# Kernel optimization log

Hardware: AMD Instinct MI355X
Metric: run time of the kernel (lower is better)

The kernel has to match this reference:

```python
import jax, jax.numpy as jnp
import numpy as np

B, T, N, E = 32, 512, 4, 16          # batch, seq_len, num_nodes, num_edges (N*N)
NI, EI = 16, 8                        # node / edge input channels
HN, HE, MH, C = 128, 128, 256, 8      # hidden node/edge, mlp hidden, classes

# complete-graph edge list (matches the src/dst double loop in __init__)
SRC = np.repeat(np.arange(N), N)      # [E]
DST = np.tile(np.arange(N), N)        # [E]
# GCNConv (PyG default) adds self-loops on top of the existing complete graph
# -> adjacency counts: off-diag 1, diag 2; in-degree of every node = N+1.
# symmetric norm deg^-1/2 A deg^-1/2 collapses to A/(N+1). Dense 4x4 matmul
# per graph is the efficient faithful form of the scatter-add here.
NORM_ADJ = (np.ones((N, N), np.float32) + np.eye(N, dtype=np.float32)) / (N + 1)


def lstm(x, Wih, Whh, b):
    """batch_first LSTM, torch gate order (i,f,g,o). x: [Bn,T,D] -> [Bn,T,H]."""
    H = Whh.shape[0]
    xz = x @ Wih + b  # precompute input projection [Bn,T,4H]

    def step(carry, zt):
        h, c = carry
        z = zt + h @ Whh
        i, f, g, o = jnp.split(z, 4, axis=-1)
        c = jax.nn.sigmoid(f) * c + jax.nn.sigmoid(i) * jnp.tanh(g)
        h = jax.nn.sigmoid(o) * jnp.tanh(c)
        return (h, c), h

    init = (jnp.zeros((x.shape[0], H), x.dtype), jnp.zeros((x.shape[0], H), x.dtype))
    _, hs = jax.lax.scan(step, init, jnp.swapaxes(xz, 0, 1))
    return jnp.swapaxes(hs, 0, 1)


def setup_inputs() -> dict:
    key = jax.random.key(0)
    ks = jax.random.split(key, 30)

    def p(k, shape, s=0.05):
        return (jax.random.normal(k, shape, jnp.float32) * s)

    return {
        "x_seq": jax.random.normal(ks[0], (B, T, N, NI), jnp.float32),
        "edge_attr_seq": jax.random.normal(ks[1], (B, T, E, EI), jnp.float32),
        "Wn1": p(ks[2], (NI, HN)), "bn1": p(ks[3], (HN,)),
        "Wn2": p(ks[4], (HN, HN)), "bn2": p(ks[5], (HN,)),
        "We1": p(ks[6], (EI, HE)), "be1": p(ks[7], (HE,)),
        "We2": p(ks[8], (HE, HE)), "be2": p(ks[9], (HE,)),
        "Wg1": p(ks[10], (HN, HN)), "bg1": p(ks[11], (HN,)),
        "Wg2": p(ks[12], (HN, HN)), "bg2": p(ks[13], (HN,)),
        "Wef1": p(ks[14], (HE, HE)), "bef1": p(ks[15], (HE,)),
        "Wef2": p(ks[16], (HE, HE)), "bef2": p(ks[17], (HE,)),
        "Wih_n": p(ks[18], (HN, 4 * HN)), "Whh_n": p(ks[19], (HN, 4 * HN)), "b_n": p(ks[20], (4 * HN,)),
        "Wih_e": p(ks[21], (HE, 4 * HE)), "Whh_e": p(ks[22], (HE, 4 * HE)), "b_e": p(ks[23], (4 * HE,)),
        "Wc1": p(ks[24], (2 * HN + HE, MH)), "bc1": p(ks[25], (MH,)),
        "Wc2": p(ks[26], (MH, C)), "bc2": p(ks[27], (C,)),
    }


def reference(x_seq, edge_attr_seq, Wn1, bn1, Wn2, bn2, We1, be1, We2, be2,
              Wg1, bg1, Wg2, bg2, Wef1, bef1, Wef2, bef2,
              Wih_n, Whh_n, b_n, Wih_e, Whh_e, b_e, Wc1, bc1, Wc2, bc2):
    adj = jnp.asarray(NORM_ADJ)
    # node / edge MLP embeddings
    x = jax.nn.relu(jax.nn.relu(x_seq @ Wn1 + bn1) @ Wn2 + bn2)      # [B,T,N,HN]
    e = jax.nn.relu(jax.nn.relu(edge_attr_seq @ We1 + be1) @ We2 + be2)  # [B,T,E,HE]
    # two GCN layers: normalized-adjacency aggregation per (batch,time) graph
    x = jax.nn.relu(jnp.einsum('ij,btjd->btid', adj, x @ Wg1) + bg1)
    x = jax.nn.relu(jnp.einsum('ij,btjd->btid', adj, x @ Wg2) + bg2)
    # edge FC stack
    e = jax.nn.relu(jax.nn.relu(e @ Wef1 + bef1) @ Wef2 + bef2)
    # LSTMs over time, one sequence per (batch, node) / (batch, edge)
    xn = x.transpose(0, 2, 1, 3).reshape(B * N, T, HN)
    en = e.transpose(0, 2, 1, 3).reshape(B * E, T, HE)
    hn = lstm(xn, Wih_n, Whh_n, b_n).reshape(B, N, T, HN).transpose(0, 2, 1, 3)  # [B,T,N,HN]
    he = lstm(en, Wih_e, Whh_e, b_e).reshape(B, E, T, HE).transpose(0, 2, 1, 3)  # [B,T,E,HE]
    # edge-gather classifier
    src_f = hn[:, :, jnp.asarray(SRC), :]
    dst_f = hn[:, :, jnp.asarray(DST), :]
    feats = jnp.concatenate([src_f, dst_f, he], axis=-1)  # [B,T,E,2HN+HE]
    logits = jax.nn.relu(feats @ Wc1 + bc1) @ Wc2 + bc2   # [B,T,E,C]
    return logits
```

## Files before the change

kernel.cpp:

```cpp
#include <hip/hip_runtime.h>
#include <cstdint>

constexpr int T_  = 512;
constexpr int HN_ = 128;

#define DEVI __device__ __forceinline__

typedef __bf16 bf16x8 __attribute__((ext_vector_type(8)));
typedef __bf16 bf16x4 __attribute__((ext_vector_type(4)));
typedef __bf16 bf16x2 __attribute__((ext_vector_type(2)));
typedef float  f32x4  __attribute__((ext_vector_type(4)));

DEVI float sigf(float x) { return __builtin_amdgcn_rcpf(1.f + __expf(-x)); }
DEVI float tanh_fast(float x) {
  x = fminf(fmaxf(x, -15.f), 15.f);
  return 1.f - 2.f * __builtin_amdgcn_rcpf(1.f + __expf(2.f * x));
}
DEVI float swz_xor8(float x) {
  return __int_as_float(__builtin_amdgcn_ds_swizzle(__float_as_int(x), 0x201F));
}

DEVI void layer128_bf(const __bf16* __restrict__ src, __bf16* __restrict__ dst,
                      bf16x8 w0, bf16x8 w1, bf16x8 w2, bf16x8 w3,
                      float bv, int lm, int lh, int n)
{
  #pragma unroll
  for (int m = 0; m < 4; ++m) {
    const __bf16* sp = &src[(m*16 + lm)*136 + lh*8];
    const bf16x8 a0 = *reinterpret_cast<const bf16x8*>(sp);
    const bf16x8 a1 = *reinterpret_cast<const bf16x8*>(sp + 32);
    const bf16x8 a2 = *reinterpret_cast<const bf16x8*>(sp + 64);
    const bf16x8 a3 = *reinterpret_cast<const bf16x8*>(sp + 96);
    f32x4 acc = { bv, bv, bv, bv };
    acc = __builtin_amdgcn_mfma_f32_16x16x32_bf16(a0, w0, acc, 0, 0, 0);
    acc = __builtin_amdgcn_mfma_f32_16x16x32_bf16(a1, w1, acc, 0, 0, 0);
    acc = __builtin_amdgcn_mfma_f32_16x16x32_bf16(a2, w2, acc, 0, 0, 0);
    acc = __builtin_amdgcn_mfma_f32_16x16x32_bf16(a3, w3, acc, 0, 0, 0);
    #pragma unroll
    for (int r = 0; r < 4; ++r)
      dst[(m*16 + lh*4 + r)*136 + n] = (__bf16)fmaxf(acc[r], 0.f);
  }
}

DEVI void layer128_f32(const __bf16* __restrict__ src, float* __restrict__ dst,
                       bf16x8 w0, bf16x8 w1, bf16x8 w2, bf16x8 w3,
                       float bv, bool relu, int lm, int lh, int n)
{
  #pragma unroll
  for (int m = 0; m < 4; ++m) {
    const __bf16* sp = &src[(m*16 + lm)*136 + lh*8];
    const bf16x8 a0 = *reinterpret_cast<const bf16x8*>(sp);
    const bf16x8 a1 = *reinterpret_cast<const bf16x8*>(sp + 32);
    const bf16x8 a2 = *reinterpret_cast<const bf16x8*>(sp + 64);
    const bf16x8 a3 = *reinterpret_cast<const bf16x8*>(sp + 96);
    f32x4 acc = { bv, bv, bv, bv };
    acc = __builtin_amdgcn_mfma_f32_16x16x32_bf16(a0, w0, acc, 0, 0, 0);
    acc = __builtin_amdgcn_mfma_f32_16x16x32_bf16(a1, w1, acc, 0, 0, 0);
    acc = __builtin_amdgcn_mfma_f32_16x16x32_bf16(a2, w2, acc, 0, 0, 0);
    acc = __builtin_amdgcn_mfma_f32_16x16x32_bf16(a3, w3, acc, 0, 0, 0);
    #pragma unroll
    for (int r = 0; r < 4; ++r)
      dst[(m*16 + lh*4 + r)*132 + n] = relu ? fmaxf(acc[r], 0.f) : acc[r];
  }
}

__global__ __launch_bounds__(512, 4) void node_mlp_mfma_kernel(
    const float* __restrict__ x_seq,
    const float* __restrict__ Wn1, const float* __restrict__ bn1,
    const float* __restrict__ Wn2, const float* __restrict__ bn2,
    const float* __restrict__ Wg1, const float* __restrict__ bg1,
    const float* __restrict__ Wg2, const float* __restrict__ bg2,
    float* __restrict__ xn)
{
  constexpr int P1 = 40;
  __shared__ __align__(16) __bf16 A1[64 * P1];
  __shared__ __align__(16) __bf16 Ab[64 * 136];
  __shared__ __align__(16) __bf16 Bb[64 * 136];
  __shared__ __align__(16) float  Yf[64 * 132];

  const int tid = threadIdx.x;
  const int w = tid >> 6, l = tid & 63, lm = l & 15, lh = l >> 4;
  const int n = w*16 + lm;

  bf16x8 w1, w2[4], w3[4], w4[4];
  const float b1 = bn1[n], b2 = bn2[n];
  #pragma unroll
  for (int j = 0; j < 8; ++j) {
    const int k = lh*8 + j;
    w1[j] = (k < 16) ? (__bf16)Wn1[k*128 + n] : (__bf16)0.f;
  }
  #pragma unroll
  for (int kt = 0; kt < 4; ++kt)
    #pragma unroll
    for (int j = 0; j < 8; ++j) {
      const int k = kt*32 + lh*8 + j;
      w2[kt][j] = (__bf16)Wn2[k*128 + n];
      w3[kt][j] = (__bf16)Wg1[k*128 + n];
      w4[kt][j] = (__bf16)Wg2[k*128 + n];
    }

  for (int i = tid; i < 64 * P1; i += 512) A1[i] = (__bf16)0.f;

  for (int g = blockIdx.x; g < 1024; g += 512) {
    #pragma unroll
    for (int it = 0; it < 2; ++it) {
      const int i = tid + it*512;
      A1[(i >> 4)*P1 + (i & 15)] = (__bf16)x_seq[(size_t)g*1024 + i];
    }
    __syncthreads();
    #pragma unroll
    for (int m = 0; m < 4; ++m) {
      const bf16x8 a = *reinterpret_cast<const bf16x8*>(&A1[(m*16+lm)*P1 + lh*8]);
      f32x4 acc = { b1, b1, b1, b1 };
      acc = __builtin_amdgcn_mfma_f32_16x16x32_bf16(a, w1, acc, 0, 0, 0);
      #pragma unroll
      for (int r = 0; r < 4; ++r)
        Ab[(m*16 + lh*4 + r)*136 + n] = (__bf16)fmaxf(acc[r], 0.f);
    }
    __syncthreads();
    layer128_bf(Ab, Bb, w2[0], w2[1], w2[2], w2[3], b2, lm, lh, n);
    __syncthreads();
    layer128_f32(Bb, Yf, w3[0], w3[1], w3[2], w3[3], 0.f, false, lm, lh, n);
    __syncthreads();
    #pragma unroll
    for (int it = 0; it < 4; ++it) {
      const int idx = tid + it*512;
      const int q = idx >> 7, d = idx & 127;
      const float y0 = Yf[(q*4+0)*132 + d], y1 = Yf[(q*4+1)*132 + d];
      const float y2 = Yf[(q*4+2)*132 + d], y3 = Yf[(q*4+3)*132 + d];
      const float s = y0 + y1 + y2 + y3;
      const float bv = bg1[d];
      Ab[(q*4+0)*136 + d] = (__bf16)fmaxf((s + y0)*0.2f + bv, 0.f);
      Ab[(q*4+1)*136 + d] = (__bf16)fmaxf((s + y1)*0.2f + bv, 0.f);
      Ab[(q*4+2)*136 + d] = (__bf16)fmaxf((s + y2)*0.2f + bv, 0.f);
      Ab[(q*4+3)*136 + d] = (__bf16)fmaxf((s + y3)*0.2f + bv, 0.f);
    }
    __syncthreads();
    layer128_f32(Ab, Yf, w4[0], w4[1], w4[2], w4[3], 0.f, false, lm, lh, n);
    __syncthreads();
    #pragma unroll
    for (int it = 0; it < 4; ++it) {
      const int idx = tid + it*512;
      const int q = idx >> 7, d = idx & 127;
      const int bt = g*16 + q, bb = bt >> 9, tt = bt & 511;
      const float y0 = Yf[(q*4+0)*132 + d], y1 = Yf[(q*4+1)*132 + d];
      const float y2 = Yf[(q*4+2)*132 + d], y3 = Yf[(q*4+3)*132 + d];
      const float s = y0 + y1 + y2 + y3;
      const float bv = bg2[d];
      xn[((size_t)(bb*4+0)*T_ + tt)*HN_ + d] = fmaxf((s + y0)*0.2f + bv, 0.f);
      xn[((size_t)(bb*4+1)*T_ + tt)*HN_ + d] = fmaxf((s + y1)*0.2f + bv, 0.f);
      xn[((size_t)(bb*4+2)*T_ + tt)*HN_ + d] = fmaxf((s + y2)*0.2f + bv, 0.f);
      xn[((size_t)(bb*4+3)*T_ + tt)*HN_ + d] = fmaxf((s + y3)*0.2f + bv, 0.f);
    }
    __syncthreads();
  }
}

__global__ __launch_bounds__(512, 4) void edge_mlp_mfma_kernel(
    const float* __restrict__ ea,
    const float* __restrict__ We1, const float* __restrict__ be1,
    const float* __restrict__ We2, const float* __restrict__ be2,
    const float* __restrict__ Wef1, const float* __restrict__ bef1,
    const float* __restrict__ Wef2, const float* __restrict__ bef2,
    float* __restrict__ en)
{
  constexpr int P1 = 40;
  __shared__ __align__(16) __bf16 A1[64 * P1];
  __shared__ __align__(16) __bf16 Ab[64 * 136];
  __shared__ __align__(16) __bf16 Bb[64 * 136];
  __shared__ __align__(16) float  Of[64 * 132];

  const int tid = threadIdx.x;
  const int w = tid >> 6, l = tid & 63, lm = l & 15, lh = l >> 4;
  const int n = w*16 + lm;

  bf16x8 w1, w2[4], w3[4], w4[4];
  const float b1 = be1[n], b2 = be2[n], b3 = bef1[n], b4 = bef2[n];
  #pragma unroll
  for (int j = 0; j < 8; ++j) {
    const int k = lh*8 + j;
    w1[j] = (k < 8) ? (__bf16)We1[k*128 + n] : (__bf16)0.f;
  }
  #pragma unroll
  for (int kt = 0; kt < 4; ++kt)
    #pragma unroll
    for (int j = 0; j < 8; ++j) {
      const int k = kt*32 + lh*8 + j;
      w2[kt][j] = (__bf16)We2[k*128 + n];
      w3[kt][j] = (__bf16)Wef1[k*128 + n];
      w4[kt][j] = (__bf16)Wef2[k*128 + n];
    }

  for (int i = tid; i < 64 * P1; i += 512) A1[i] = (__bf16)0.f;

  for (int g = blockIdx.x; g < 4096; g += 512) {
    A1[(tid >> 3)*P1 + (tid & 7)] = (__bf16)ea[(size_t)g*512 + tid];
    __syncthreads();
    #pragma unroll
    for (int m = 0; m < 4; ++m) {
      const bf16x8 a = *reinterpret_cast<const bf16x8*>(&A1[(m*16+lm)*P1 + lh*8]);
      f32x4 acc = { b1, b1, b1, b1 };
      acc = __builtin_amdgcn_mfma_f32_16x16x32_bf16(a, w1, acc, 0, 0, 0);
      #pragma unroll
      for (int r = 0; r < 4; ++r)
        Ab[(m*16 + lh*4 + r)*136 + n] = (__bf16)fmaxf(acc[r], 0.f);
    }
    __syncthreads();
    layer128_bf(Ab, Bb, w2[0], w2[1], w2[2], w2[3], b2, lm, lh, n);
    __syncthreads();
    layer128_bf(Bb, Ab, w3[0], w3[1], w3[2], w3[3], b3, lm, lh, n);
    __syncthreads();
    layer128_f32(Ab, Of, w4[0], w4[1], w4[2], w4[3], b4, true, lm, lh, n);
    __syncthreads();
    #pragma unroll
    for (int i = 0; i < 4; ++i) {
      const int fi = tid + i*512;
      const int row = fi >> 5, c4 = fi & 31;
      const int q = row >> 4, e = row & 15;
      const int bt = g*4 + q, bb = bt >> 9, tt = bt & 511;
      const float4 v = *reinterpret_cast<const float4*>(&Of[row*132 + c4*4]);
      *reinterpret_cast<float4*>(
          &en[((size_t)(bb*16+e)*T_ + tt)*HN_ + c4*4]) = v;
    }
    __syncthreads();
  }
}

__global__ __launch_bounds__(512, 1) void lstm_mfma_kernel(
    const float* __restrict__ Wih_n, const float* __restrict__ Whh_n,
    const float* __restrict__ b_n,
    const float* __restrict__ Wih_e, const float* __restrict__ Whh_e,
    const float* __restrict__ b_e,
    float* __restrict__ xn, float* __restrict__ en)
{
  __shared__ __align__(16) __bf16 x_c[8 * 2048];
  __shared__ __align__(16) __bf16 x_zero[2048];
  __shared__ __align__(16) __bf16 h_bf[8 * 128];
  __shared__ __align__(16) __bf16 h_zero[128];
  __shared__ __align__(16) float  h_hist[8 * 2048];

  const bool is_node = (int)blockIdx.x < 16;
  const int  bidx    = is_node ? blockIdx.x : ((int)blockIdx.x - 16);
  const float* __restrict__ Wih  = is_node ? Wih_n : Wih_e;
  const float* __restrict__ Whh  = is_node ? Whh_n : Whh_e;
  const float* __restrict__ bias = is_node ? b_n   : b_e;
  float* __restrict__ xh = (is_node ? xn : en) + (size_t)bidx * 8 * (T_ * HN_);

  const int tid = threadIdx.x;
  const int w   = tid >> 6;
  const int l   = tid & 63;
  const int lm  = l & 15;
  const int lh  = l >> 4;

  bf16x8 wih_f[4][4], whh_f[4][4];
  f32x4  bias_v[4];
  #pragma unroll
  for (int nt = 0; nt < 4; ++nt) {
    const int g0 = nt*128 + w*16;
    bias_v[nt] = *reinterpret_cast<const f32x4*>(&bias[g0 + lh*4]);
    #pragma unroll
    for (int kt = 0; kt < 4; ++kt) {
      #pragma unroll
      for (int j = 0; j < 8; ++j) {
        const int k = kt*32 + lh*8 + j;
        wih_f[nt][kt][j] = (__bf16)Wih[k*512 + g0 + lm];
        whh_f[nt][kt][j] = (__bf16)Whh[k*512 + g0 + lm];
      }
    }
  }

  for (int i = tid; i < 2048; i += 512) x_zero[i] = (__bf16)0.f;
  for (int i = tid; i < 8 * 128; i += 512) h_bf[i] = (__bf16)0.f;
  if (tid < 128) h_zero[tid] = (__bf16)0.f;

  const int swz = (lm < 8) ? ((lm & 7) << 4) : 0;
  const __bf16* __restrict__ xrow = (lm < 8) ? &x_c[lm * 2048] : x_zero;
  const __bf16* __restrict__ hrow = (lm < 8) ? &h_bf[lm * 128] : h_zero;
  int foff[4];
  #pragma unroll
  for (int kt = 0; kt < 4; ++kt)
    foff[kt] = ((kt*64 + lh*16) ^ swz) >> 1;

  const bool hi_half = lm >= 8;
  const int  s  = lm & 7;
  const int hb_unit = (2*w + (lh >> 1)) ^ s;
  const int hb_idx  = s*128 + (((hb_unit << 4) + 8*(lh & 1) + (hi_half ? 4 : 0)) >> 1);
  const int hh_col  = (w*4 + lh) ^ s;
  const int hh_base = s*2048 + hh_col*4 + (hi_half ? 2 : 0);
  float c0 = 0.f, c1 = 0.f;

  bf16x8 bx[4];
  for (int t = 0; t < T_; ++t) {
    const int tl = t & 15;
    if (tl == 0) {
      if (t) {
        #pragma unroll
        for (int i = 0; i < 8; ++i) {
          const int tl2 = tid >> 5, u = tid & 31;
          const float4 v = *reinterpret_cast<const float4*>(
              &h_hist[i*2048 + (tid ^ (i & 7))*4]);
          *reinterpret_cast<float4*>(
              &xh[(size_t)i*(T_*HN_) + (size_t)(t-16+tl2)*HN_ + u*4]) = v;
        }
      }
      #pragma unroll
      for (int i = 0; i < 8; ++i) {
        const float4 v = *reinterpret_cast<const float4*>(
            &xh[(size_t)i*(T_*HN_) + (size_t)t*HN_ + tid*4]);
        bf16x4 pk;
        pk[0] = (__bf16)v.x; pk[1] = (__bf16)v.y;
        pk[2] = (__bf16)v.z; pk[3] = (__bf16)v.w;
        *reinterpret_cast<bf16x4*>(
            &x_c[i*2048 + (((tid >> 1) ^ (i & 7)) << 3) + (tid & 1)*4]) = pk;
      }
      __syncthreads();
      #pragma unroll
      for (int kt = 0; kt < 4; ++kt)
        bx[kt] = *reinterpret_cast<const bf16x8*>(&xrow[foff[kt]]);
    }

    bf16x8 bh[4];
    #pragma unroll
    for (int kt = 0; kt < 4; ++kt)
      bh[kt] = *reinterpret_cast<const bf16x8*>(&hrow[foff[kt]]);

    f32x4 accs[4];
    #pragma unroll
    for (int nt = 0; nt < 4; ++nt) {
      f32x4 aA = bias_v[nt];
      f32x4 aB = { 0.f, 0.f, 0.f, 0.f };
      #pragma unroll
      for (int kt = 0; kt < 4; ++kt) {
        aA = __builtin_amdgcn_mfma_f32_16x16x32_bf16(wih_f[nt][kt], bx[kt], aA, 0, 0, 0);
        aB = __builtin_amdgcn_mfma_f32_16x16x32_bf16(whh_f[nt][kt], bh[kt], aB, 0, 0, 0);
      }
      accs[nt] = aA + aB;
    }

    if (tl != 15) {
      #pragma unroll
      for (int kt = 0; kt < 4; ++kt)
        bx[kt] = *reinterpret_cast<const bf16x8*>(&xrow[(tl+1)*128 + foff[kt]]);
    }

    float z0[4], z1[4];
    #pragma unroll
    for (int nt = 0; nt < 4; ++nt) {
      const float a2 = swz_xor8(accs[nt][2]);
      const float a3 = swz_xor8(accs[nt][3]);
      z0[nt] = hi_half ? a2 : accs[nt][0];
      z1[nt] = hi_half ? a3 : accs[nt][1];
    }
    c0 = sigf(z0[1]) * c0 + sigf(z0[0]) * tanh_fast(z0[2]);
    const float h0 = sigf(z0[3]) * tanh_fast(c0);
    c1 = sigf(z1[1]) * c1 + sigf(z1[0]) * tanh_fast(z1[2]);
    const float h1 = sigf(z1[3]) * tanh_fast(c1);

    bf16x2 hb; hb[0] = (__bf16)h0; hb[1] = (__bf16)h1;
    *reinterpret_cast<bf16x2*>(&h_bf[hb_idx]) = hb;
    float2 ho; ho.x = h0; ho.y = h1;
    *reinterpret_cast<float2*>(&h_hist[hh_base + tl*128]) = ho;
    __syncthreads();
  }
  #pragma unroll
  for (int i = 0; i < 8; ++i) {
    const int tl2 = tid >> 5, u = tid & 31;
    const float4 v = *reinterpret_cast<const float4*>(
        &h_hist[i*2048 + (tid ^ (i & 7))*4]);
    *reinterpret_cast<float4*>(
        &xh[(size_t)i*(T_*HN_) + (size_t)(T_-16+tl2)*HN_ + u*4]) = v;
  }
}

__global__ __launch_bounds__(512, 1) void classifier_mfma_kernel(
    const float* __restrict__ hn, const float* __restrict__ he,
    const float* __restrict__ Wc1, const float* __restrict__ bc1,
    const float* __restrict__ Wc2, const float* __restrict__ bc2,
    float* __restrict__ out)
{
  constexpr int HP = 136;
  constexpr int DP = 264;
  __shared__ __align__(16) __bf16 hn_l[32 * HP];
  __shared__ __align__(16) __bf16 he_l[128 * HP];
  __shared__ __align__(16) __bf16 hid_l[128 * DP];

  const int tid = threadIdx.x;
  const int w   = tid >> 6;
  const int l   = tid & 63;
  const int lm  = l & 15;
  const int lh  = l >> 4;

  bf16x8 wb[2][12];
  float  bcol[2];
  #pragma unroll
  for (int jt = 0; jt < 2; ++jt) {
    const int j = w*32 + jt*16 + lm;
    bcol[jt] = bc1[j];
    #pragma unroll
    for (int kt = 0; kt < 12; ++kt)
      #pragma unroll
      for (int i = 0; i < 8; ++i)
        wb[jt][kt][i] = (__bf16)Wc1[(kt*32 + lh*8 + i)*256 + j];
  }
  bf16x8 wc2f[8];
  const float bc2v = (lm < 8) ? bc2[lm] : 0.f;
  #pragma unroll
  for (int kt = 0; kt < 8; ++kt)
    #pragma unroll
    for (int i = 0; i < 8; ++i)
      wc2f[kt][i] = (lm < 8) ? (__bf16)Wc2[(kt*32 + lh*8 + i)*8 + lm] : (__bf16)0.f;

  for (int g = blockIdx.x; g < 2048; g += 256) {
    const int b  = g >> 6;
    const int t0 = (g & 63) * 8;

    for (int i = tid; i < 4096; i += 512) {
      const int f4 = i * 4;
      const int e  = f4 >> 10;
      const int rem = f4 & 1023;
      const int tt = rem >> 7;
      const int k  = rem & 127;
      const float4 v = *reinterpret_cast<const float4*>(
          &he[((size_t)(b*16+e)*T_ + t0 + tt)*HN_ + k]);
      __bf16* p = &he_l[(tt*16 + e)*HP + k];
      p[0]=(__bf16)v.x; p[1]=(__bf16)v.y; p[2]=(__bf16)v.z; p[3]=(__bf16)v.w;
    }
    for (int i = tid; i < 1024; i += 512) {
      const int f4 = i * 4;
      const int n  = f4 >> 10;
      const int rem = f4 & 1023;
      const int tt = rem >> 7;
      const int k  = rem & 127;
      const float4 v = *reinterpret_cast<const float4*>(
          &hn[((size_t)(b*4+n)*T_ + t0 + tt)*HN_ + k]);
      __bf16* p = &hn_l[(tt*4 + n)*HP + k];
      p[0]=(__bf16)v.x; p[1]=(__bf16)v.y; p[2]=(__bf16)v.z; p[3]=(__bf16)v.w;
    }
    __syncthreads();

    for (int tt = 0; tt < 8; ++tt) {
      bf16x8 af[12];
      #pragma unroll
      for (int kt = 0; kt < 4; ++kt)
        af[kt] = *reinterpret_cast<const bf16x8*>(
            &hn_l[(tt*4 + (lm>>2))*HP + kt*32 + lh*8]);
      #pragma unroll
      for (int kt = 0; kt < 4; ++kt)
        af[4+kt] = *reinterpret_cast<const bf16x8*>(
            &hn_l[(tt*4 + (lm&3))*HP + kt*32 + lh*8]);
      #pragma unroll
      for (int kt = 0; kt < 4; ++kt)
        af[8+kt] = *reinterpret_cast<const bf16x8*>(
            &he_l[(tt*16 + lm)*HP + kt*32 + lh*8]);
      #pragma unroll
      for (int jt = 0; jt < 2; ++jt) {
        f32x4 acc = { bcol[jt], bcol[jt], bcol[jt], bcol[jt] };
        #pragma unroll
        for (int kt = 0; kt < 12; ++kt)
          acc = __builtin_amdgcn_mfma_f32_16x16x32_bf16(af[kt], wb[jt][kt], acc, 0, 0, 0);
        #pragma unroll
        for (int r = 0; r < 4; ++r)
          hid_l[(tt*16 + lh*4 + r)*DP + (w*2 + jt)*16 + lm] = (__bf16)fmaxf(acc[r], 0.f);
      }
    }
    __syncthreads();

    {
      const int tt = w;
      f32x4 acc = { bc2v, bc2v, bc2v, bc2v };
      #pragma unroll
      for (int kt = 0; kt < 8; ++kt) {
        const bf16x8 a = *reinterpret_cast<const bf16x8*>(
            &hid_l[(tt*16 + lm)*DP + kt*32 + lh*8]);
        acc = __builtin_amdgcn_mfma_f32_16x16x32_bf16(a, wc2f[kt], acc, 0, 0, 0);
      }
      if (lm < 8) {
        const size_t bt = (size_t)b*T_ + t0 + tt;
        #pragma unroll
        for (int r = 0; r < 4; ++r)
          out[(bt*16 + lh*4 + r)*8 + lm] = acc[r];
      }
    }
    __syncthreads();
  }
}

extern "C" void kernel_launch(void* const* d_in, const int* in_sizes, int n_in,
                              void* d_out, int out_size, void* d_ws, size_t ws_size,
                              hipStream_t stream) {
  (void)in_sizes; (void)n_in; (void)out_size; (void)ws_size;
  const float* x_seq = (const float*)d_in[0];
  const float* ea    = (const float*)d_in[1];
  const float* Wn1 = (const float*)d_in[2];
  const float* bn1 = (const float*)d_in[3];
  const float* Wn2 = (const float*)d_in[4];
  const float* bn2 = (const float*)d_in[5];
  const float* We1 = (const float*)d_in[6];
  const float* be1 = (const float*)d_in[7];
  const float* We2 = (const float*)d_in[8];
  const float* be2 = (const float*)d_in[9];
  const float* Wg1 = (const float*)d_in[10];
  const float* bg1 = (const float*)d_in[11];
  const float* Wg2 = (const float*)d_in[12];
  const float* bg2 = (const float*)d_in[13];
  const float* Wef1 = (const float*)d_in[14];
  const float* bef1 = (const float*)d_in[15];
  const float* Wef2 = (const float*)d_in[16];
  const float* bef2 = (const float*)d_in[17];
  const float* Wih_n = (const float*)d_in[18];
  const float* Whh_n = (const float*)d_in[19];
  const float* b_n   = (const float*)d_in[20];
  const float* Wih_e = (const float*)d_in[21];
  const float* Whh_e = (const float*)d_in[22];
  const float* b_e   = (const float*)d_in[23];
  const float* Wc1 = (const float*)d_in[24];
  const float* bc1 = (const float*)d_in[25];
  const float* Wc2 = (const float*)d_in[26];
  const float* bc2 = (const float*)d_in[27];

  float* xn = (float*)d_ws;
  float* en = xn + (size_t)128 * T_ * HN_;
  float* out = (float*)d_out;

  node_mlp_mfma_kernel<<<512, 512, 0, stream>>>(x_seq, Wn1, bn1, Wn2, bn2,
                                                Wg1, bg1, Wg2, bg2, xn);
  edge_mlp_mfma_kernel<<<512, 512, 0, stream>>>(ea, We1, be1, We2, be2,
                                                Wef1, bef1, Wef2, bef2, en);
  lstm_mfma_kernel<<<80, 512, 0, stream>>>(Wih_n, Whh_n, b_n,
                                           Wih_e, Whh_e, b_e, xn, en);
  classifier_mfma_kernel<<<256, 512, 0, stream>>>(xn, en, Wc1, bc1, Wc2, bc2, out);
}
```

Measured before the change: 827.1 us.

## Store intermediates in bf16 and restructure LSTM to 16 sequences per block

Intermediate node/edge activations and LSTM outputs are now stored in the workspace as bf16 instead of fp32, which halves global traffic between kernels and lets the classifier copy them without converting. The LSTM kernel is rebuilt. Each block now processes 16 sequences, so the MFMA N dimension is fully used and the grid shrinks from 80 to 40 blocks. Gate columns are permuted so each lane holds i,f,g,o for its own unit, which removes the cross-lane swizzle. The input projection for the next step is software-pipelined with register double-buffering from global memory, and h history goes into a 16-step LDS ring that is flushed every 16 steps. This trades some precision and serial work per block (fewer blocks, more per-step MFMA) for better MFMA utilization and less memory traffic. The tanh input clamp is also removed.

Result: faster. 779.5 us (-5.7%).

```diff
diff --git a/kernel.cpp b/kernel.cpp
--- a/kernel.cpp
+++ b/kernel.cpp
@@ -8,16 +8,11 @@
 
 typedef __bf16 bf16x8 __attribute__((ext_vector_type(8)));
 typedef __bf16 bf16x4 __attribute__((ext_vector_type(4)));
-typedef __bf16 bf16x2 __attribute__((ext_vector_type(2)));
 typedef float  f32x4  __attribute__((ext_vector_type(4)));
 
 DEVI float sigf(float x) { return __builtin_amdgcn_rcpf(1.f + __expf(-x)); }
 DEVI float tanh_fast(float x) {
-  x = fminf(fmaxf(x, -15.f), 15.f);
   return 1.f - 2.f * __builtin_amdgcn_rcpf(1.f + __expf(2.f * x));
-}
-DEVI float swz_xor8(float x) {
-  return __int_as_float(__builtin_amdgcn_ds_swizzle(__float_as_int(x), 0x201F));
 }
 
 DEVI void layer128_bf(const __bf16* __restrict__ src, __bf16* __restrict__ dst,
@@ -70,7 +65,7 @@
     const float* __restrict__ Wn2, const float* __restrict__ bn2,
     const float* __restrict__ Wg1, const float* __restrict__ bg1,
     const float* __restrict__ Wg2, const float* __restrict__ bg2,
-    float* __restrict__ xn)
+    __bf16* __restrict__ xn)
 {
   constexpr int P1 = 40;
   __shared__ __align__(16) __bf16 A1[64 * P1];
@@ -147,10 +142,10 @@
       const float y2 = Yf[(q*4+2)*132 + d], y3 = Yf[(q*4+3)*132 + d];
       const float s = y0 + y1 + y2 + y3;
       const float bv = bg2[d];
-      xn[((size_t)(bb*4+0)*T_ + tt)*HN_ + d] = fmaxf((s + y0)*0.2f + bv, 0.f);
-      xn[((size_t)(bb*4+1)*T_ + tt)*HN_ + d] = fmaxf((s + y1)*0.2f + bv, 0.f);
-      xn[((size_t)(bb*4+2)*T_ + tt)*HN_ + d] = fmaxf((s + y2)*0.2f + bv, 0.f);
-      xn[((size_t)(bb*4+3)*T_ + tt)*HN_ + d] = fmaxf((s + y3)*0.2f + bv, 0.f);
+      xn[((size_t)(bb*4+0)*T_ + tt)*HN_ + d] = (__bf16)fmaxf((s + y0)*0.2f + bv, 0.f);
+      xn[((size_t)(bb*4+1)*T_ + tt)*HN_ + d] = (__bf16)fmaxf((s + y1)*0.2f + bv, 0.f);
+      xn[((size_t)(bb*4+2)*T_ + tt)*HN_ + d] = (__bf16)fmaxf((s + y2)*0.2f + bv, 0.f);
+      xn[((size_t)(bb*4+3)*T_ + tt)*HN_ + d] = (__bf16)fmaxf((s + y3)*0.2f + bv, 0.f);
     }
     __syncthreads();
   }
@@ -162,7 +157,7 @@
     const float* __restrict__ We2, const float* __restrict__ be2,
     const float* __restrict__ Wef1, const float* __restrict__ bef1,
     const float* __restrict__ Wef2, const float* __restrict__ bef2,
-    float* __restrict__ en)
+    __bf16* __restrict__ en)
 {
   constexpr int P1 = 40;
   __shared__ __align__(16) __bf16 A1[64 * P1];
@@ -219,32 +214,30 @@
       const int q = row >> 4, e = row & 15;
       const int bt = g*4 + q, bb = bt >> 9, tt = bt & 511;
       const float4 v = *reinterpret_cast<const float4*>(&Of[row*132 + c4*4]);
-      *reinterpret_cast<float4*>(
-          &en[((size_t)(bb*16+e)*T_ + tt)*HN_ + c4*4]) = v;
-    }
-    __syncthreads();
-  }
-}
-
-__global__ __launch_bounds__(512, 1) void lstm_mfma_kernel(
+      bf16x4 pk;
+      pk[0]=(__bf16)v.x; pk[1]=(__bf16)v.y; pk[2]=(__bf16)v.z; pk[3]=(__bf16)v.w;
+      *reinterpret_cast<bf16x4*>(
+          &en[((size_t)(bb*16+e)*T_ + tt)*HN_ + c4*4]) = pk;
+    }
+    __syncthreads();
+  }
+}
+
+__global__ __launch_bounds__(512, 2) void lstm_mfma_kernel(
     const float* __restrict__ Wih_n, const float* __restrict__ Whh_n,
     const float* __restrict__ b_n,
     const float* __restrict__ Wih_e, const float* __restrict__ Whh_e,
     const float* __restrict__ b_e,
-    float* __restrict__ xn, float* __restrict__ en)
+    __bf16* __restrict__ xn, __bf16* __restrict__ en)
 {
-  __shared__ __align__(16) __bf16 x_c[8 * 2048];
-  __shared__ __align__(16) __bf16 x_zero[2048];
-  __shared__ __align__(16) __bf16 h_bf[8 * 128];
-  __shared__ __align__(16) __bf16 h_zero[128];
-  __shared__ __align__(16) float  h_hist[8 * 2048];
-
-  const bool is_node = (int)blockIdx.x < 16;
-  const int  bidx    = is_node ? blockIdx.x : ((int)blockIdx.x - 16);
+  __shared__ __align__(16) __bf16 ring[16 * 16 * 128];
+
+  const bool is_node = (int)blockIdx.x < 8;
+  const int  bidx    = is_node ? blockIdx.x : ((int)blockIdx.x - 8);
   const float* __restrict__ Wih  = is_node ? Wih_n : Wih_e;
   const float* __restrict__ Whh  = is_node ? Whh_n : Whh_e;
   const float* __restrict__ bias = is_node ? b_n   : b_e;
-  float* __restrict__ xh = (is_node ? xn : en) + (size_t)bidx * 8 * (T_ * HN_);
+  __bf16* __restrict__ xh = (is_node ? xn : en) + (size_t)bidx * 16 * (T_ * HN_);
 
   const int tid = threadIdx.x;
   const int w   = tid >> 6;
@@ -256,124 +249,116 @@
   f32x4  bias_v[4];
   #pragma unroll
   for (int nt = 0; nt < 4; ++nt) {
-    const int g0 = nt*128 + w*16;
-    bias_v[nt] = *reinterpret_cast<const f32x4*>(&bias[g0 + lh*4]);
-    #pragma unroll
-    for (int kt = 0; kt < 4; ++kt) {
+    const int d   = w*16 + nt*4 + lh;
+    bias_v[nt][0] = bias[0*128 + d];
+    bias_v[nt][1] = bias[1*128 + d];
+    bias_v[nt][2] = bias[2*128 + d];
+    bias_v[nt][3] = bias[3*128 + d];
+    const int col = (lm & 3)*128 + w*16 + nt*4 + (lm >> 2);
+    #pragma unroll
+    for (int kt = 0; kt < 4; ++kt)
       #pragma unroll
       for (int j = 0; j < 8; ++j) {
         const int k = kt*32 + lh*8 + j;
-        wih_f[nt][kt][j] = (__bf16)Wih[k*512 + g0 + lm];
-        whh_f[nt][kt][j] = (__bf16)Whh[k*512 + g0 + lm];
+        wih_f[nt][kt][j] = (__bf16)Wih[k*512 + col];
+        whh_f[nt][kt][j] = (__bf16)Whh[k*512 + col];
       }
-    }
-  }
-
-  for (int i = tid; i < 2048; i += 512) x_zero[i] = (__bf16)0.f;
-  for (int i = tid; i < 8 * 128; i += 512) h_bf[i] = (__bf16)0.f;
-  if (tid < 128) h_zero[tid] = (__bf16)0.f;
-
-  const int swz = (lm < 8) ? ((lm & 7) << 4) : 0;
-  const __bf16* __restrict__ xrow = (lm < 8) ? &x_c[lm * 2048] : x_zero;
-  const __bf16* __restrict__ hrow = (lm < 8) ? &h_bf[lm * 128] : h_zero;
-  int foff[4];
+  }
+
+  {
+    bf16x4 z; z[0]=z[1]=z[2]=z[3]=(__bf16)0.f;
+    *reinterpret_cast<bf16x4*>(&ring[15*2048 + tid*4]) = z;
+  }
+  __syncthreads();
+
+  const size_t seqStride = (size_t)T_ * HN_;
+  const __bf16* __restrict__ xseq = xh + (size_t)lm * seqStride;
+
+  f32x4 accsX[4];
+  {
+    bf16x8 bx[4];
+    #pragma unroll
+    for (int kt = 0; kt < 4; ++kt)
+      bx[kt] = *reinterpret_cast<const bf16x8*>(&xseq[kt*32 + lh*8]);
+    #pragma unroll
+    for (int nt = 0; nt < 4; ++nt) {
+      accsX[nt] = bias_v[nt];
+      #pragma unroll
+      for (int kt = 0; kt < 4; ++kt)
+        accsX[nt] = __builtin_amdgcn_mfma_f32_16x16x32_bf16(wih_f[nt][kt], bx[kt], accsX[nt], 0, 0, 0);
+    }
+  }
+  bf16x8 bxO[4], bxE[4];
   #pragma unroll
   for (int kt = 0; kt < 4; ++kt)
-    foff[kt] = ((kt*64 + lh*16) ^ swz) >> 1;
-
-  const bool hi_half = lm >= 8;
-  const int  s  = lm & 7;
-  const int hb_unit = (2*w + (lh >> 1)) ^ s;
-  const int hb_idx  = s*128 + (((hb_unit << 4) + 8*(lh & 1) + (hi_half ? 4 : 0)) >> 1);
-  const int hh_col  = (w*4 + lh) ^ s;
-  const int hh_base = s*2048 + hh_col*4 + (hi_half ? 2 : 0);
-  float c0 = 0.f, c1 = 0.f;
-
-  bf16x8 bx[4];
+    bxO[kt] = *reinterpret_cast<const bf16x8*>(&xseq[(size_t)1*HN_ + kt*32 + lh*8]);
+
+  float c[4] = {0.f, 0.f, 0.f, 0.f};
+
+  #pragma unroll 2
   for (int t = 0; t < T_; ++t) {
-    const int tl = t & 15;
-    if (tl == 0) {
-      if (t) {
-        #pragma unroll
-        for (int i = 0; i < 8; ++i) {
-          const int tl2 = tid >> 5, u = tid & 31;
-          const float4 v = *reinterpret_cast<const float4*>(
-              &h_hist[i*2048 + (tid ^ (i & 7))*4]);
-          *reinterpret_cast<float4*>(
-              &xh[(size_t)i*(T_*HN_) + (size_t)(t-16+tl2)*HN_ + u*4]) = v;
-        }
-      }
+    bf16x8* bxLoad = (t & 1) ? bxO : bxE;
+    bf16x8* bxUse  = (t & 1) ? bxE : bxO;
+    {
+      const int tp = (t + 2 < T_) ? t + 2 : T_ - 1;
+      #pragma unroll
+      for (int kt = 0; kt < 4; ++kt)
+        bxLoad[kt] = *reinterpret_cast<const bf16x8*>(
+            &xseq[(size_t)tp*HN_ + kt*32 + lh*8]);
+    }
+
+    const int rbase = ((t + 15) & 15)*2048 + lm*128;
+    bf16x8 bh[4];
+    #pragma unroll
+    for (int kt = 0; kt < 4; ++kt)
+      bh[kt] = *reinterpret_cast<const bf16x8*>(
+          &ring[rbase + (((kt*4 + lh) ^ (lm & 7)) << 3)]);
+
+    #pragma unroll
+    for (int nt = 0; nt < 4; ++nt)
+      #pragma unroll
+      for (int kt = 0; kt < 4; ++kt)
+        accsX[nt] = __builtin_amdgcn_mfma_f32_16x16x32_bf16(whh_f[nt][kt], bh[kt], accsX[nt], 0, 0, 0);
+
+    const int wbase = (t & 15)*2048 + lm*128;
+    #pragma unroll
+    for (int nt = 0; nt < 4; ++nt) {
+      const float zi = accsX[nt][0], zf = accsX[nt][1];
+      const float zg = accsX[nt][2], zo = accsX[nt][3];
+      c[nt] = sigf(zf)*c[nt] + sigf(zi)*tanh_fast(zg);
+      const float h = sigf(zo)*tanh_fast(c[nt]);
+      const int up = (2*w + (nt >> 1)) ^ (lm & 7);
+      ring[wbase + up*8 + (nt & 1)*4 + lh] = (__bf16)h;
+    }
+
+    #pragma unroll
+    for (int nt = 0; nt < 4; ++nt) {
+      accsX[nt] = bias_v[nt];
+      #pragma unroll
+      for (int kt = 0; kt < 4; ++kt)
+        accsX[nt] = __builtin_amdgcn_mfma_f32_16x16x32_bf16(wih_f[nt][kt], bxUse[kt], accsX[nt], 0, 0, 0);
+    }
+    __syncthreads();
+
+    if ((t & 15) == 15) {
+      const int tb = t - 15;
       #pragma unroll
       for (int i = 0; i < 8; ++i) {
-        const float4 v = *reinterpret_cast<const float4*>(
-            &xh[(size_t)i*(T_*HN_) + (size_t)t*HN_ + tid*4]);
-        bf16x4 pk;
-        pk[0] = (__bf16)v.x; pk[1] = (__bf16)v.y;
-        pk[2] = (__bf16)v.z; pk[3] = (__bf16)v.w;
-        *reinterpret_cast<bf16x4*>(
-            &x_c[i*2048 + (((tid >> 1) ^ (i & 7)) << 3) + (tid & 1)*4]) = pk;
+        const int uf = tid + i*512;
+        const int tl = uf >> 8, sq = (uf >> 4) & 15, us = uf & 15;
+        const int ulog = us ^ (sq & 7);
+        const bf16x8 v = *reinterpret_cast<const bf16x8*>(
+            &ring[tl*2048 + sq*128 + us*8]);
+        *reinterpret_cast<bf16x8*>(
+            &xh[(size_t)sq*seqStride + (size_t)(tb + tl)*HN_ + ulog*8]) = v;
       }
       __syncthreads();
-      #pragma unroll
-      for (int kt = 0; kt < 4; ++kt)
-        bx[kt] = *reinterpret_cast<const bf16x8*>(&xrow[foff[kt]]);
-    }
-
-    bf16x8 bh[4];
-    #pragma unroll
-    for (int kt = 0; kt < 4; ++kt)
-      bh[kt] = *reinterpret_cast<const bf16x8*>(&hrow[foff[kt]]);
-
-    f32x4 accs[4];
-    #pragma unroll
-    for (int nt = 0; nt < 4; ++nt) {
-      f32x4 aA = bias_v[nt];
-      f32x4 aB = { 0.f, 0.f, 0.f, 0.f };
-      #pragma unroll
-      for (int kt = 0; kt < 4; ++kt) {
-        aA = __builtin_amdgcn_mfma_f32_16x16x32_bf16(wih_f[nt][kt], bx[kt], aA, 0, 0, 0);
-        aB = __builtin_amdgcn_mfma_f32_16x16x32_bf16(whh_f[nt][kt], bh[kt], aB, 0, 0, 0);
-      }
-      accs[nt] = aA + aB;
-    }
-
-    if (tl != 15) {
-      #pragma unroll
-      for (int kt = 0; kt < 4; ++kt)
-        bx[kt] = *reinterpret_cast<const bf16x8*>(&xrow[(tl+1)*128 + foff[kt]]);
-    }
-
-    float z0[4], z1[4];
-    #pragma unroll
-    for (int nt = 0; nt < 4; ++nt) {
-      const float a2 = swz_xor8(accs[nt][2]);
-      const float a3 = swz_xor8(accs[nt][3]);
-      z0[nt] = hi_half ? a2 : accs[nt][0];
-      z1[nt] = hi_half ? a3 : accs[nt][1];
-    }
-    c0 = sigf(z0[1]) * c0 + sigf(z0[0]) * tanh_fast(z0[2]);
-    const float h0 = sigf(z0[3]) * tanh_fast(c0);
-    c1 = sigf(z1[1]) * c1 + sigf(z1[0]) * tanh_fast(z1[2]);
-    const float h1 = sigf(z1[3]) * tanh_fast(c1);
-
-    bf16x2 hb; hb[0] = (__bf16)h0; hb[1] = (__bf16)h1;
-    *reinterpret_cast<bf16x2*>(&h_bf[hb_idx]) = hb;
-    float2 ho; ho.x = h0; ho.y = h1;
-    *reinterpret_cast<float2*>(&h_hist[hh_base + tl*128]) = ho;
-    __syncthreads();
-  }
-  #pragma unroll
-  for (int i = 0; i < 8; ++i) {
-    const int tl2 = tid >> 5, u = tid & 31;
-    const float4 v = *reinterpret_cast<const float4*>(
-        &h_hist[i*2048 + (tid ^ (i & 7))*4]);
-    *reinterpret_cast<float4*>(
-        &xh[(size_t)i*(T_*HN_) + (size_t)(T_-16+tl2)*HN_ + u*4]) = v;
+    }
   }
 }
 
 __global__ __launch_bounds__(512, 1) void classifier_mfma_kernel(
-    const float* __restrict__ hn, const float* __restrict__ he,
+    const __bf16* __restrict__ hn, const __bf16* __restrict__ he,
     const float* __restrict__ Wc1, const float* __restrict__ bc1,
     const float* __restrict__ Wc2, const float* __restrict__ bc2,
     float* __restrict__ out)
@@ -414,27 +399,19 @@
     const int b  = g >> 6;
     const int t0 = (g & 63) * 8;
 
-    for (int i = tid; i < 4096; i += 512) {
-      const int f4 = i * 4;
-      const int e  = f4 >> 10;
-      const int rem = f4 & 1023;
-      const int tt = rem >> 7;
-      const int k  = rem & 127;
-      const float4 v = *reinterpret_cast<const float4*>(
+    for (int u = tid; u < 2048; u += 512) {
+      const int e = u >> 7, rem = u & 127;
+      const int tt = rem >> 4, k = (rem & 15)*8;
+      const bf16x8 v = *reinterpret_cast<const bf16x8*>(
           &he[((size_t)(b*16+e)*T_ + t0 + tt)*HN_ + k]);
-      __bf16* p = &he_l[(tt*16 + e)*HP + k];
-      p[0]=(__bf16)v.x; p[1]=(__bf16)v.y; p[2]=(__bf16)v.z; p[3]=(__bf16)v.w;
-    }
-    for (int i = tid; i < 1024; i += 512) {
-      const int f4 = i * 4;
-      const int n  = f4 >> 10;
-      const int rem = f4 & 1023;
-      const int tt = rem >> 7;
-      const int k  = rem & 127;
-      const float4 v = *reinterpret_cast<const float4*>(
+      *reinterpret_cast<bf16x8*>(&he_l[(tt*16 + e)*HP + k]) = v;
+    }
+    for (int u = tid; u < 512; u += 512) {
+      const int n = u >> 7, rem = u & 127;
+      const int tt = rem >> 4, k = (rem & 15)*8;
+      const bf16x8 v = *reinterpret_cast<const bf16x8*>(
           &hn[((size_t)(b*4+n)*T_ + t0 + tt)*HN_ + k]);
-      __bf16* p = &hn_l[(tt*4 + n)*HP + k];
-      p[0]=(__bf16)v.x; p[1]=(__bf16)v.y; p[2]=(__bf16)v.z; p[3]=(__bf16)v.w;
+      *reinterpret_cast<bf16x8*>(&hn_l[(tt*4 + n)*HP + k]) = v;
     }
     __syncthreads();
 
@@ -518,15 +495,15 @@
   const float* Wc2 = (const float*)d_in[26];
   const float* bc2 = (const float*)d_in[27];
 
-  float* xn = (float*)d_ws;
-  float* en = xn + (size_t)128 * T_ * HN_;
+  __bf16* xn = (__bf16*)d_ws;
+  __bf16* en = xn + (size_t)128 * T_ * HN_;
   float* out = (float*)d_out;
 
   node_mlp_mfma_kernel<<<512, 512, 0, stream>>>(x_seq, Wn1, bn1, Wn2, bn2,
                                                 Wg1, bg1, Wg2, bg2, xn);
   edge_mlp_mfma_kernel<<<512, 512, 0, stream>>>(ea, We1, be1, We2, be2,
                                                 Wef1, bef1, Wef2, bef2, en);
-  lstm_mfma_kernel<<<80, 512, 0, stream>>>(Wih_n, Whh_n, b_n,
+  lstm_mfma_kernel<<<40, 512, 0, stream>>>(Wih_n, Whh_n, b_n,
                                            Wih_e, Whh_e, b_e, xn, en);
   classifier_mfma_kernel<<<256, 512, 0, stream>>>(xn, en, Wc1, bc1, Wc2, bc2, out);
 }
```
